# Optimization experiments

Hardware: AMD Instinct MI355X
Metric: run time of the kernel (lower is better)

Reference implementation:

```python
import jax, jax.numpy as jnp
import numpy as np

E = 8          # num_local_experts
D = 1024       # hidden_size
F = 4096       # intermediate_size_moe
T = 2048       # tokens (seq_len)
K = 2          # num_experts_per_tok


def setup_inputs() -> dict:
    key = jax.random.key(0)
    k_x, k_r, k_g, k_u, k_d = jax.random.split(key, 5)
    s = lambda fan_in: 1.0 / np.sqrt(fan_in)
    return {
        "x_TD": jax.random.normal(k_x, (T, D), dtype=jnp.float32),
        "w_router_DE": jax.random.normal(k_r, (D, E), dtype=jnp.float32) * s(D),
        "kernel_gating_EDF": jax.random.normal(k_g, (E, D, F), dtype=jnp.float32) * s(D),
        "kernel_up_proj_EDF": jax.random.normal(k_u, (E, D, F), dtype=jnp.float32) * s(D),
        "kernel_down_proj_EFD": jax.random.normal(k_d, (E, F, D), dtype=jnp.float32) * s(F),
    }


def reference(x_TD, w_router_DE, kernel_gating_EDF, kernel_up_proj_EDF, kernel_down_proj_EFD):
    # --- Router: softmax -> top-k -> renormalize ---
    logits_TE = x_TD @ w_router_DE                       # [T, E]
    probs_TE = jax.nn.softmax(logits_TE, axis=-1)
    topk_vals, topk_idx = jax.lax.top_k(probs_TE, K)     # [T, K]
    topk_vals = topk_vals / jnp.sum(topk_vals, axis=-1, keepdims=True)  # renormalize=True
    # Dense combine weights: scatter top-k weights back to [T, E]
    weights_TE = jnp.sum(
        jax.nn.one_hot(topk_idx, E, dtype=x_TD.dtype) * topk_vals[..., None], axis=1
    )

    # --- Dense-mat expert MLP (SwiGLU), all experts for all tokens ---
    gate_TEF = jnp.einsum("td,edf->tef", x_TD, kernel_gating_EDF)
    up_TEF = jnp.einsum("td,edf->tef", x_TD, kernel_up_proj_EDF)
    h_TEF = jax.nn.silu(gate_TEF) * up_TEF

    # Down-project each expert and combine weighted by router
    # (apply_expert_weight_before_computation=False -> weight applied at combine)
    out_TD = jnp.einsum("tef,efd,te->td", h_TEF, kernel_down_proj_EFD, weights_TE)
    return out_TD
```

## Files before the change

### kernel.cpp

```cpp
#include <hip/hip_runtime.h>
#include <hip/hip_bf16.h>
#include <math.h>

#define T_TOK 2048
#define D_DIM 1024
#define F_DIM 4096
#define E_NUM 8

typedef __attribute__((ext_vector_type(8))) short short8;
typedef __attribute__((ext_vector_type(4))) short short4v;
typedef __attribute__((ext_vector_type(4))) float floatx4;

__device__ __forceinline__ short f2bf(float f) {
  union { float f; unsigned u; } v; v.f = f;
  unsigned r = v.u + 0x7fffu + ((v.u >> 16) & 1u);
  return (short)(r >> 16);
}

__device__ __forceinline__ void gld_lds16(const void* g, void* l) {
  __builtin_amdgcn_global_load_lds(
      (const __attribute__((address_space(1))) unsigned int*)g,
      (__attribute__((address_space(3))) unsigned int*)l, 16, 0, 0);
}

__global__ __launch_bounds__(256) void router_kernel(
    const float* __restrict__ x, const float* __restrict__ wr,
    int* __restrict__ counts, int* __restrict__ slot_sid, float* __restrict__ slot_w) {
  int lane = threadIdx.x & 63;
  int wave = threadIdx.x >> 6;
  int t = blockIdx.x * 4 + wave;
  const float* xr = x + (size_t)t * D_DIM;
  float acc[8];
#pragma unroll
  for (int e = 0; e < 8; e++) acc[e] = 0.f;
#pragma unroll
  for (int i = 0; i < 16; i++) {
    int d = i * 64 + lane;
    float xv = xr[d];
    const float* w = wr + d * 8;
    float4 w0 = *(const float4*)(w);
    float4 w1 = *(const float4*)(w + 4);
    acc[0] += xv * w0.x; acc[1] += xv * w0.y;
    acc[2] += xv * w0.z; acc[3] += xv * w0.w;
    acc[4] += xv * w1.x; acc[5] += xv * w1.y;
    acc[6] += xv * w1.z; acc[7] += xv * w1.w;
  }
#pragma unroll
  for (int off = 32; off > 0; off >>= 1) {
#pragma unroll
    for (int e = 0; e < 8; e++) acc[e] += __shfl_xor(acc[e], off, 64);
  }
  if (lane == 0) {
    int e1 = 0; float l1 = acc[0];
#pragma unroll
    for (int e = 1; e < 8; e++) { if (acc[e] > l1) { l1 = acc[e]; e1 = e; } }
    int e2 = -1; float l2 = -3.4e38f;
#pragma unroll
    for (int e = 0; e < 8; e++) { if (e != e1 && acc[e] > l2) { l2 = acc[e]; e2 = e; } }
    float w1 = 1.f / (1.f + __expf(l2 - l1));
    float w2 = 1.f - w1;
    int p1 = atomicAdd(&counts[e1], 1);
    slot_sid[e1 * T_TOK + p1] = 2 * t;
    slot_w[e1 * T_TOK + p1] = w1;
    int p2 = atomicAdd(&counts[e2], 1);
    slot_sid[e2 * T_TOK + p2] = 2 * t + 1;
    slot_w[e2 * T_TOK + p2] = w2;
  }
}

__global__ __launch_bounds__(256) void cvt_x_kernel(const float* __restrict__ x,
                                                    short* __restrict__ Xb) {
  int i = blockIdx.x * 256 + threadIdx.x;
  float4 v = ((const float4*)x)[i];
  short4v s;
  s[0] = f2bf(v.x); s[1] = f2bf(v.y); s[2] = f2bf(v.z); s[3] = f2bf(v.w);
  ((short4v*)Xb)[i] = s;
}

__global__ __launch_bounds__(256) void transpose_cvt_kernel(
    const float* __restrict__ src, short* __restrict__ dst, int R, int C) {
  __shared__ short tile[64][68];
  int cb = blockIdx.x * 64, rb = blockIdx.y * 64;
  size_t plane = (size_t)blockIdx.z * R * C;
  src += plane; dst += plane;
  int tid = threadIdx.x;
  int r0 = tid >> 4, c4 = (tid & 15) * 4;
#pragma unroll
  for (int i = 0; i < 4; i++) {
    int r = r0 + i * 16;
    float4 v = *(const float4*)&src[(size_t)(rb + r) * C + cb + c4];
    short4v s;
    s[0] = f2bf(v.x); s[1] = f2bf(v.y); s[2] = f2bf(v.z); s[3] = f2bf(v.w);
    *(short4v*)&tile[r][c4] = s;
  }
  __syncthreads();
  int c0 = tid >> 4, r4 = (tid & 15) * 4;
#pragma unroll
  for (int i = 0; i < 4; i++) {
    int c = c0 + i * 16;
    short4v s;
    s[0] = tile[r4][c]; s[1] = tile[r4 + 1][c];
    s[2] = tile[r4 + 2][c]; s[3] = tile[r4 + 3][c];
    *(short4v*)&dst[(size_t)(cb + c) * R + rb + r4] = s;
  }
}

__global__ __launch_bounds__(256, 2) void gateup_kernel(
    const short* __restrict__ Xb, const short* __restrict__ WgT, const short* __restrict__ WuT,
    const int* __restrict__ counts, const int* __restrict__ slot_sid,
    short* __restrict__ H) {
  __shared__ short smem[3 * 4096];
  short* As = smem;
  short* Bg = smem + 4096;
  short* Bu = smem + 8192;
  __shared__ int s_sid[128];

  int bid = blockIdx.x;
  int nt = bid & 31;
  int mt = (bid >> 5) & 15;
  int e  = bid >> 9;
  int n_e = counts[e];
  if (mt * 128 >= n_e) return;

  int tid = threadIdx.x;
  if (tid < 128) {
    int i = mt * 128 + tid;
    if (i > n_e - 1) i = n_e - 1;
    s_sid[tid] = slot_sid[e * T_TOK + i];
  }
  __syncthreads();

  int lane = tid & 63;
  int w = tid >> 6;
  int wm = w >> 1, wn = w & 1;
  int r16 = lane & 15, q = lane >> 4;

  int srow0 = w * 32 + (lane >> 2);
  int srow1 = srow0 + 16;
  int kc = (lane & 3) * 8;
  const short* aP0 = Xb + (size_t)(s_sid[srow0] >> 1) * D_DIM + kc;
  const short* aP1 = Xb + (size_t)(s_sid[srow1] >> 1) * D_DIM + kc;
  size_t wbase = (size_t)e * F_DIM * D_DIM + (size_t)(nt * 128) * D_DIM;
  const short* gP0 = WgT + wbase + (size_t)srow0 * D_DIM + kc;
  const short* gP1 = WgT + wbase + (size_t)srow1 * D_DIM + kc;
  const short* uP0 = WuT + wbase + (size_t)srow0 * D_DIM + kc;
  const short* uP1 = WuT + wbase + (size_t)srow1 * D_DIM + kc;
  short* lds0 = (short*)smem + (w * 32) * 32;
  short* lds1 = (short*)smem + (w * 32 + 16) * 32;

  floatx4 zero4 = {0.f, 0.f, 0.f, 0.f};
  floatx4 accg[4][4], accu[4][4];
#pragma unroll
  for (int a = 0; a < 4; a++)
#pragma unroll
    for (int b = 0; b < 4; b++) { accg[a][b] = zero4; accu[a][b] = zero4; }

  for (int kb = 0; kb < D_DIM / 32; kb++) {
    gld_lds16(aP0, lds0);
    gld_lds16(aP1, lds1);
    gld_lds16(gP0, lds0 + 4096);
    gld_lds16(gP1, lds1 + 4096);
    gld_lds16(uP0, lds0 + 8192);
    gld_lds16(uP1, lds1 + 8192);
    aP0 += 32; aP1 += 32; gP0 += 32; gP1 += 32; uP0 += 32; uP1 += 32;
    __syncthreads();
    short8 af[4], bgf[4], buf_[4];
#pragma unroll
    for (int f = 0; f < 4; f++) {
      af[f]   = *(const short8*)&As[(wm * 64 + f * 16 + r16) * 32 + q * 8];
      bgf[f]  = *(const short8*)&Bg[(wn * 64 + f * 16 + r16) * 32 + q * 8];
      buf_[f] = *(const short8*)&Bu[(wn * 64 + f * 16 + r16) * 32 + q * 8];
    }
#pragma unroll
    for (int fm = 0; fm < 4; fm++)
#pragma unroll
      for (int fn = 0; fn < 4; fn++) {
        accg[fm][fn] = __builtin_amdgcn_mfma_f32_16x16x32_bf16(af[fm], bgf[fn],  accg[fm][fn], 0, 0, 0);
        accu[fm][fn] = __builtin_amdgcn_mfma_f32_16x16x32_bf16(af[fm], buf_[fn], accu[fm][fn], 0, 0, 0);
      }
    __syncthreads();
  }

  short* slab = smem;
#pragma unroll
  for (int fm = 0; fm < 4; fm++) {
#pragma unroll
    for (int reg = 0; reg < 4; reg++) {
      int rowl = wm * 16 + q * 4 + reg;
#pragma unroll
      for (int fn = 0; fn < 4; fn++) {
        float g = accg[fm][fn][reg];
        float u = accu[fm][fn][reg];
        float h = g * u / (1.f + __expf(-g));
        slab[rowl * 136 + wn * 64 + fn * 16 + r16] = f2bf(h);
      }
    }
    __syncthreads();
    int rl = tid >> 3, cs = (tid & 7) * 16;
    int grow = (rl >> 4) * 64 + fm * 16 + (rl & 15);
    if (mt * 128 + grow < n_e) {
      int sid = s_sid[grow];
      short8 v0 = *(const short8*)&slab[rl * 136 + cs];
      short8 v1 = *(const short8*)&slab[rl * 136 + cs + 8];
      short* hp = H + (size_t)sid * F_DIM + nt * 128 + cs;
      *(short8*)&hp[0] = v0;
      *(short8*)&hp[8] = v1;
    }
    __syncthreads();
  }
}

__global__ __launch_bounds__(256, 3) void down_kernel(
    const short* __restrict__ H, const short* __restrict__ WdT,
    const int* __restrict__ counts, const int* __restrict__ slot_sid,
    const float* __restrict__ slot_w, float* __restrict__ Y) {
  __shared__ short smem[2 * 4096];
  short* As = smem;
  short* Bs = smem + 4096;
  __shared__ int s_sid[128];
  __shared__ float s_w[128];

  int bid = blockIdx.x;
  int nt = bid & 7;
  int sk = (bid >> 3) & 3;
  int mt = (bid >> 5) & 15;
  int e  = bid >> 9;
  int n_e = counts[e];
  if (mt * 128 >= n_e) return;

  int tid = threadIdx.x;
  if (tid < 128) {
    int i = mt * 128 + tid;
    if (i > n_e - 1) i = n_e - 1;
    s_sid[tid] = slot_sid[e * T_TOK + i];
    s_w[tid]   = slot_w[e * T_TOK + i];
  }
  __syncthreads();

  int lane = tid & 63;
  int w = tid >> 6;
  int wm = w >> 1, wn = w & 1;
  int r16 = lane & 15, q = lane >> 4;

  int srow0 = w * 32 + (lane >> 2);
  int srow1 = srow0 + 16;
  int kc = (lane & 3) * 8;
  int ks = sk * (F_DIM / 4);
  const short* aP0 = H + (size_t)s_sid[srow0] * F_DIM + ks + kc;
  const short* aP1 = H + (size_t)s_sid[srow1] * F_DIM + ks + kc;
  size_t wbase = ((size_t)e * D_DIM + nt * 128) * F_DIM;
  const short* bP0 = WdT + wbase + (size_t)srow0 * F_DIM + ks + kc;
  const short* bP1 = WdT + wbase + (size_t)srow1 * F_DIM + ks + kc;
  short* lds0 = smem + (w * 32) * 32;
  short* lds1 = smem + (w * 32 + 16) * 32;

  floatx4 zero4 = {0.f, 0.f, 0.f, 0.f};
  floatx4 acc[4][4];
#pragma unroll
  for (int a = 0; a < 4; a++)
#pragma unroll
    for (int b = 0; b < 4; b++) acc[a][b] = zero4;

  for (int kb = 0; kb < (F_DIM / 4) / 32; kb++) {
    gld_lds16(aP0, lds0);
    gld_lds16(aP1, lds1);
    gld_lds16(bP0, lds0 + 4096);
    gld_lds16(bP1, lds1 + 4096);
    aP0 += 32; aP1 += 32; bP0 += 32; bP1 += 32;
    __syncthreads();
    short8 af[4], bf[4];
#pragma unroll
    for (int f = 0; f < 4; f++) {
      af[f] = *(const short8*)&As[(wm * 64 + f * 16 + r16) * 32 + q * 8];
      bf[f] = *(const short8*)&Bs[(wn * 64 + f * 16 + r16) * 32 + q * 8];
    }
#pragma unroll
    for (int fm = 0; fm < 4; fm++)
#pragma unroll
      for (int fn = 0; fn < 4; fn++)
        acc[fm][fn] = __builtin_amdgcn_mfma_f32_16x16x32_bf16(af[fm], bf[fn], acc[fm][fn], 0, 0, 0);
    __syncthreads();
  }

#pragma unroll
  for (int fm = 0; fm < 4; fm++) {
#pragma unroll
    for (int reg = 0; reg < 4; reg++) {
      int row = wm * 64 + fm * 16 + q * 4 + reg;
      int i = mt * 128 + row;
      if (i < n_e) {
        int sid = s_sid[row];
        float wgt = s_w[row];
        float* yp = Y + ((size_t)sk * (T_TOK * 2) + sid) * D_DIM + nt * 128 + wn * 64 + r16;
#pragma unroll
        for (int fn = 0; fn < 4; fn++)
          yp[fn * 16] = acc[fm][fn][reg] * wgt;
      }
    }
  }
}

__global__ __launch_bounds__(256) void combine_kernel(
    const float* __restrict__ Y, float* __restrict__ out) {
  int idx = blockIdx.x * 256 + threadIdx.x;
  int t = idx >> 8;
  int j = idx & 255;
  const floatx4* Yv = (const floatx4*)Y;
  floatx4 s = {0.f, 0.f, 0.f, 0.f};
#pragma unroll
  for (int sk = 0; sk < 4; sk++) {
    s += Yv[((size_t)sk * (T_TOK * 2) + 2 * t) * 256 + j];
    s += Yv[((size_t)sk * (T_TOK * 2) + 2 * t + 1) * 256 + j];
  }
  ((floatx4*)out)[idx] = s;
}

extern "C" void kernel_launch(void* const* d_in, const int* in_sizes, int n_in,
                              void* d_out, int out_size, void* d_ws, size_t ws_size,
                              hipStream_t stream) {
  const float* x  = (const float*)d_in[0];
  const float* wr = (const float*)d_in[1];
  const float* Wg = (const float*)d_in[2];
  const float* Wu = (const float*)d_in[3];
  const float* Wd = (const float*)d_in[4];
  float* out = (float*)d_out;

  char* ws = (char*)d_ws;
  int*   counts   = (int*)(ws);
  int*   slot_sid = (int*)(ws + 4096);
  float* slot_w   = (float*)(ws + 4096 + 65536);
  short* Xb       = (short*)(ws + 0x40000);
  short* H        = (short*)(ws + 0x800000);
  short* WgT      = (short*)(ws + 0x2800000);
  short* WuT      = (short*)(ws + 0x6800000);
  short* WdT      = WgT;
  float* Y4       = (float*)WuT;

  hipMemsetAsync(counts, 0, E_NUM * sizeof(int), stream);
  router_kernel<<<T_TOK / 4, 256, 0, stream>>>(x, wr, counts, slot_sid, slot_w);
  cvt_x_kernel<<<T_TOK * D_DIM / 4 / 256, 256, 0, stream>>>(x, Xb);
  transpose_cvt_kernel<<<dim3(F_DIM / 64, D_DIM / 64, E_NUM), 256, 0, stream>>>(Wg, WgT, D_DIM, F_DIM);
  transpose_cvt_kernel<<<dim3(F_DIM / 64, D_DIM / 64, E_NUM), 256, 0, stream>>>(Wu, WuT, D_DIM, F_DIM);
  gateup_kernel<<<E_NUM * 32 * 16, 256, 0, stream>>>(Xb, WgT, WuT, counts, slot_sid, H);
  transpose_cvt_kernel<<<dim3(D_DIM / 64, F_DIM / 64, E_NUM), 256, 0, stream>>>(Wd, WdT, F_DIM, D_DIM);
  down_kernel<<<E_NUM * 8 * 4 * 16, 256, 0, stream>>>(H, WdT, counts, slot_sid, slot_w, Y4);
  combine_kernel<<<T_TOK * D_DIM / 4 / 256, 256, 0, stream>>>(Y4, out);
}
```

Baseline: 645.3 us.

## Double-buffer LDS tiles in gate/up and down GEMM kernels to overlap loads

Both expert GEMM kernels now keep two LDS buffers and prefetch the next K-slice with direct global-to-LDS loads while MFMAs run on the current slice. Partial vmcnt waits plus raw s_barrier and sched_barrier calls replace the old load-then-sync-then-compute sequence. The aim is to hide global memory latency behind compute. In exchange, LDS use per block doubles (48KB for gate/up, 32KB for down), which may reduce how many blocks fit per CU under the launch bounds.

```diff
diff --git a/kernel.cpp b/kernel.cpp
--- a/kernel.cpp
+++ b/kernel.cpp
@@ -109,10 +109,7 @@
     const short* __restrict__ Xb, const short* __restrict__ WgT, const short* __restrict__ WuT,
     const int* __restrict__ counts, const int* __restrict__ slot_sid,
     short* __restrict__ H) {
-  __shared__ short smem[3 * 4096];
-  short* As = smem;
-  short* Bg = smem + 4096;
-  short* Bu = smem + 8192;
+  __shared__ short smem[2 * 3 * 4096];
   __shared__ int s_sid[128];
 
   int bid = blockIdx.x;
@@ -145,8 +142,8 @@
   const short* gP1 = WgT + wbase + (size_t)srow1 * D_DIM + kc;
   const short* uP0 = WuT + wbase + (size_t)srow0 * D_DIM + kc;
   const short* uP1 = WuT + wbase + (size_t)srow1 * D_DIM + kc;
-  short* lds0 = (short*)smem + (w * 32) * 32;
-  short* lds1 = (short*)smem + (w * 32 + 16) * 32;
+  int ldsoff0 = (w * 32) * 32;
+  int ldsoff1 = (w * 32 + 16) * 32;
 
   floatx4 zero4 = {0.f, 0.f, 0.f, 0.f};
   floatx4 accg[4][4], accu[4][4];
@@ -155,15 +152,37 @@
 #pragma unroll
     for (int b = 0; b < 4; b++) { accg[a][b] = zero4; accu[a][b] = zero4; }
 
-  for (int kb = 0; kb < D_DIM / 32; kb++) {
-    gld_lds16(aP0, lds0);
-    gld_lds16(aP1, lds1);
-    gld_lds16(gP0, lds0 + 4096);
-    gld_lds16(gP1, lds1 + 4096);
-    gld_lds16(uP0, lds0 + 8192);
-    gld_lds16(uP1, lds1 + 8192);
+  {
+    short* n0 = smem + ldsoff0;
+    short* n1 = smem + ldsoff1;
+    gld_lds16(aP0, n0);        gld_lds16(aP1, n1);
+    gld_lds16(gP0, n0 + 4096); gld_lds16(gP1, n1 + 4096);
+    gld_lds16(uP0, n0 + 8192); gld_lds16(uP1, n1 + 8192);
     aP0 += 32; aP1 += 32; gP0 += 32; gP1 += 32; uP0 += 32; uP1 += 32;
-    __syncthreads();
+  }
+
+#pragma unroll 2
+  for (int kb = 0; kb < 32; kb++) {
+    int cur = kb & 1;
+    short* cb_ = smem + cur * 12288;
+    if (kb < 31) {
+      short* nb = smem + (cur ^ 1) * 12288;
+      short* n0 = nb + ldsoff0;
+      short* n1 = nb + ldsoff1;
+      gld_lds16(aP0, n0);        gld_lds16(aP1, n1);
+      gld_lds16(gP0, n0 + 4096); gld_lds16(gP1, n1 + 4096);
+      gld_lds16(uP0, n0 + 8192); gld_lds16(uP1, n1 + 8192);
+      aP0 += 32; aP1 += 32; gP0 += 32; gP1 += 32; uP0 += 32; uP1 += 32;
+      asm volatile("s_waitcnt vmcnt(6)" ::: "memory");
+    } else {
+      asm volatile("s_waitcnt vmcnt(0)" ::: "memory");
+    }
+    __builtin_amdgcn_s_barrier();
+    __builtin_amdgcn_sched_barrier(0);
+
+    const short* As = cb_;
+    const short* Bg = cb_ + 4096;
+    const short* Bu = cb_ + 8192;
     short8 af[4], bgf[4], buf_[4];
 #pragma unroll
     for (int f = 0; f < 4; f++) {
@@ -178,7 +197,8 @@
         accg[fm][fn] = __builtin_amdgcn_mfma_f32_16x16x32_bf16(af[fm], bgf[fn],  accg[fm][fn], 0, 0, 0);
         accu[fm][fn] = __builtin_amdgcn_mfma_f32_16x16x32_bf16(af[fm], buf_[fn], accu[fm][fn], 0, 0, 0);
       }
-    __syncthreads();
+    __builtin_amdgcn_sched_barrier(0);
+    __builtin_amdgcn_s_barrier();
   }
 
   short* slab = smem;
@@ -214,9 +234,7 @@
     const short* __restrict__ H, const short* __restrict__ WdT,
     const int* __restrict__ counts, const int* __restrict__ slot_sid,
     const float* __restrict__ slot_w, float* __restrict__ Y) {
-  __shared__ short smem[2 * 4096];
-  short* As = smem;
-  short* Bs = smem + 4096;
+  __shared__ short smem[2 * 2 * 4096];
   __shared__ int s_sid[128];
   __shared__ float s_w[128];
 
@@ -251,8 +269,8 @@
   size_t wbase = ((size_t)e * D_DIM + nt * 128) * F_DIM;
   const short* bP0 = WdT + wbase + (size_t)srow0 * F_DIM + ks + kc;
   const short* bP1 = WdT + wbase + (size_t)srow1 * F_DIM + ks + kc;
-  short* lds0 = smem + (w * 32) * 32;
-  short* lds1 = smem + (w * 32 + 16) * 32;
+  int ldsoff0 = (w * 32) * 32;
+  int ldsoff1 = (w * 32 + 16) * 32;
 
   floatx4 zero4 = {0.f, 0.f, 0.f, 0.f};
   floatx4 acc[4][4];
@@ -261,13 +279,34 @@
 #pragma unroll
     for (int b = 0; b < 4; b++) acc[a][b] = zero4;
 
+  {
+    short* n0 = smem + ldsoff0;
+    short* n1 = smem + ldsoff1;
+    gld_lds16(aP0, n0);        gld_lds16(aP1, n1);
+    gld_lds16(bP0, n0 + 4096); gld_lds16(bP1, n1 + 4096);
+    aP0 += 32; aP1 += 32; bP0 += 32; bP1 += 32;
+  }
+
+#pragma unroll 2
   for (int kb = 0; kb < (F_DIM / 4) / 32; kb++) {
-    gld_lds16(aP0, lds0);
-    gld_lds16(aP1, lds1);
-    gld_lds16(bP0, lds0 + 4096);
-    gld_lds16(bP1, lds1 + 4096);
-    aP0 += 32; aP1 += 32; bP0 += 32; bP1 += 32;
-    __syncthreads();
+    int cur = kb & 1;
+    short* cb_ = smem + cur * 8192;
+    if (kb < (F_DIM / 4) / 32 - 1) {
+      short* nb = smem + (cur ^ 1) * 8192;
+      short* n0 = nb + ldsoff0;
+      short* n1 = nb + ldsoff1;
+      gld_lds16(aP0, n0);        gld_lds16(aP1, n1);
+      gld_lds16(bP0, n0 + 4096); gld_lds16(bP1, n1 + 4096);
+      aP0 += 32; aP1 += 32; bP0 += 32; bP1 += 32;
+      asm volatile("s_waitcnt vmcnt(4)" ::: "memory");
+    } else {
+      asm volatile("s_waitcnt vmcnt(0)" ::: "memory");
+    }
+    __builtin_amdgcn_s_barrier();
+    __builtin_amdgcn_sched_barrier(0);
+
+    const short* As = cb_;
+    const short* Bs = cb_ + 4096;
     short8 af[4], bf[4];
 #pragma unroll
     for (int f = 0; f < 4; f++) {
@@ -279,7 +318,8 @@
 #pragma unroll
       for (int fn = 0; fn < 4; fn++)
         acc[fm][fn] = __builtin_amdgcn_mfma_f32_16x16x32_bf16(af[fm], bf[fn], acc[fm][fn], 0, 0, 0);
-    __syncthreads();
+    __builtin_amdgcn_sched_barrier(0);
+    __builtin_amdgcn_s_barrier();
   }
 
 #pragma unroll
```

Result: no change. 646.7 us (+0.2%).
